# Optimization experiments

Measured on AMD Instinct MI355X. Metric: run time of the kernel, lower is better.

## Reference

```python
import jax, jax.numpy as jnp
import numpy as np

B, IDF, CDF, SIZE, H, L = 32, 64, 256, 32, 8, 256
SS = SIZE * SIZE  # size*size = 1024


def setup_inputs() -> dict:
    key = jax.random.key(0)
    k1, k2, k3 = jax.random.split(key, 3)
    return {
        "weightedContext": jax.random.normal(k1, (B, IDF, SS), dtype=jnp.float32),
        "context": jax.random.normal(k2, (B, CDF, L), dtype=jnp.float32),
        # per-head conv1x1 weights: [H, size*size, cdf]
        "W": jax.random.normal(k3, (H, SS, CDF), dtype=jnp.float32) * 0.02,
        "ih": SIZE,
        "iw": SIZE,
    }


def reference(weightedContext, context, W, ih, iw):
    batch, idf = weightedContext.shape[0], weightedContext.shape[1]
    # conv1x1 per head == per-head GEMM over channel dim: [B,H,SS,L]
    sourceC = jnp.einsum("hoc,bcl->bhol", W, context)
    # attention scores: [B,H,idf,L]
    attn = jnp.einsum("bio,bhol->bhil", weightedContext, sourceC)
    # softmax over sourceL (nn.Softmax() on 2D view -> dim=1 == L here)
    attn = jax.nn.softmax(attn, axis=-1)
    # weightedContext_T summed over heads: bmm(sourceC, attn^T) -> [B,idf,SS]
    ctx_out = jnp.einsum("bhol,bhil->bio", sourceC, attn)
    ctx_out = ctx_out.reshape(batch, idf, ih, iw)
    # attnOut: per-head attn transposed [B,L,idf], summed over heads
    attn_out = jnp.sum(attn, axis=1).transpose(0, 2, 1)
    return ctx_out, attn_out
```

## Files before the change

kernel.cpp:

```cpp
#include <hip/hip_runtime.h>
#include <hip/hip_bf16.h>

#define BB 32
#define IDF 64
#define CDF 256
#define SSZ 1024
#define NH 8
#define LL 256
#define KHC 2048

typedef __attribute__((ext_vector_type(8))) _Float16 half8v;
typedef __attribute__((ext_vector_type(4))) float f32x4;

#define GLDS16(g, l) __builtin_amdgcn_global_load_lds(                        \
    (const __attribute__((address_space(1))) void*)(g),                       \
    (__attribute__((address_space(3))) void*)(l), 16, 0, 0)

#define WAIT_ENTER3(NFULL, NHALF)                                             \
  { if (ks < NSTEP - 2)                                                       \
      asm volatile("s_waitcnt vmcnt(" #NFULL ")" ::: "memory");               \
    else if (ks == NSTEP - 2)                                                 \
      asm volatile("s_waitcnt vmcnt(" #NHALF ")" ::: "memory");               \
    else                                                                      \
      asm volatile("s_waitcnt vmcnt(0)" ::: "memory");                        \
    __builtin_amdgcn_s_barrier();                                             \
    __builtin_amdgcn_sched_barrier(0); }
#define BAR_EXIT()                                                            \
  { __builtin_amdgcn_sched_barrier(0);                                        \
    __builtin_amdgcn_s_barrier();                                             \
    __builtin_amdgcn_sched_barrier(0); }
#define LDS_BAR()                                                             \
  { asm volatile("s_waitcnt lgkmcnt(0)" ::: "memory");                        \
    __builtin_amdgcn_s_barrier();                                             \
    __builtin_amdgcn_sched_barrier(0); }

__device__ inline unsigned short f2h(float x) {
  _Float16 h = (_Float16)x;
  return *reinterpret_cast<unsigned short*>(&h);
}
__device__ inline float h2f(unsigned short u) {
  _Float16 h = *reinterpret_cast<_Float16*>(&u);
  return (float)h;
}

__global__ __launch_bounds__(256) void k_prep(const float* __restrict__ wc,
                                              const float* __restrict__ W,
                                              const float* __restrict__ ctx,
                                              unsigned short* __restrict__ wc16,
                                              unsigned short* __restrict__ W16,
                                              unsigned short* __restrict__ ctx16,
                                              unsigned short* __restrict__ Wt16,
                                              unsigned short* __restrict__ cT16) {
  __shared__ float Tt[64][65];
  int blk0 = blockIdx.x;
  int t = threadIdx.x;
  if (blk0 < 6144) {
    int sel = blk0 >> 11;
    int idx = ((blk0 & 2047) * 256 + t) * 4;
    const float* src = (sel == 0) ? wc : (sel == 1) ? W : ctx;
    unsigned short* d = (sel == 0) ? wc16 : (sel == 1) ? W16 : ctx16;
    float4 v = *reinterpret_cast<const float4*>(&src[idx]);
    __align__(8) unsigned short h[4] = {f2h(v.x), f2h(v.y), f2h(v.z), f2h(v.w)};
    *reinterpret_cast<int2*>(&d[idx]) = *reinterpret_cast<int2*>(h);
  } else if (blk0 < 6656) {
    int blk = blk0 - 6144;
    int h = blk >> 6, ot = (blk >> 2) & 15, cq = blk & 3;
    int og = ot * 64, cg = cq * 64;
    int o_l = t >> 4, c4 = (t & 15) * 4;
#pragma unroll
    for (int p = 0; p < 4; ++p) {
      int o = o_l + 16 * p;
      float4 v = *reinterpret_cast<const float4*>(
          &W[((size_t)h * SSZ + og + o) * CDF + cg + c4]);
      Tt[c4 + 0][o] = v.x; Tt[c4 + 1][o] = v.y;
      Tt[c4 + 2][o] = v.z; Tt[c4 + 3][o] = v.w;
    }
    __syncthreads();
    int c_l = t >> 2;
#pragma unroll
    for (int p = 0; p < 4; ++p) {
      int o0 = ((t & 3) + 4 * p) * 4;
      __align__(8) unsigned short hv[4];
#pragma unroll
      for (int j = 0; j < 4; ++j) hv[j] = f2h(Tt[c_l][o0 + j]);
      size_t base = ((size_t)h * CDF + cg + c_l) * SSZ + og + o0;
      *reinterpret_cast<int2*>(&Wt16[base]) = *reinterpret_cast<int2*>(hv);
    }
  } else {
    int blk = blk0 - 6656;
    int b = blk >> 4, cq = (blk >> 2) & 3, lt = blk & 3;
    int cg = cq * 64, lg = lt * 64;
    int c_l = t >> 4, l4 = (t & 15) * 4;
#pragma unroll
    for (int p = 0; p < 4; ++p) {
      int c = c_l + 16 * p;
      float4 v = *reinterpret_cast<const float4*>(
          &ctx[((size_t)b * CDF + cg + c) * LL + lg + l4]);
      Tt[l4 + 0][c] = v.x; Tt[l4 + 1][c] = v.y;
      Tt[l4 + 2][c] = v.z; Tt[l4 + 3][c] = v.w;
    }
    __syncthreads();
    int l_l = t >> 2;
#pragma unroll
    for (int p = 0; p < 4; ++p) {
      int c0 = ((t & 3) + 4 * p) * 4;
      __align__(8) unsigned short hv[4];
#pragma unroll
      for (int j = 0; j < 4; ++j) hv[j] = f2h(Tt[l_l][c0 + j]);
      size_t base = ((size_t)b * LL + lg + l_l) * CDF + cg + c0;
      *reinterpret_cast<int2*>(&cT16[base]) = *reinterpret_cast<int2*>(hv);
    }
  }
}

#define BUF_SH 10240

__device__ __forceinline__ void st_p1(short* dst, const short* gA, const short* gB,
                                      int wave, int lane, int k0) {
#pragma unroll
  for (int j = 0; j < 5; ++j) {
    int inst = wave * 5 + j;
    const short* src; int toff, rb;
    if (inst < 2)       { src = gA; toff = 0;    rb = inst * 16; }
    else if (inst < 18) { src = gB; toff = 1024; rb = (inst - 2) * 16; }
    else                { src = gA; toff = 9216; rb = (inst - 18) * 16; }
    int r  = rb + (lane >> 2);
    int gc = (lane & 3) ^ ((r >> 1) & 3);
    GLDS16(src + (size_t)r * SSZ + k0 + gc * 8, dst + toff + rb * 32);
  }
}
__device__ __forceinline__ void st_pB(short* dst, const short* gB, int ld,
                                      int wave, int lane, int k0) {
#pragma unroll
  for (int j = 0; j < 4; ++j) {
    int rb = (wave * 4 + j) * 16;
    int r  = rb + (lane >> 2);
    int gc = (lane & 3) ^ ((r >> 1) & 3);
    GLDS16(gB + (size_t)r * ld + k0 + gc * 8, dst + 1024 + rb * 32);
  }
}

__global__ __launch_bounds__(256) void k123(const unsigned short* __restrict__ wc16,
                                            const unsigned short* __restrict__ Wt16,
                                            const unsigned short* __restrict__ cT16,
                                            const unsigned short* __restrict__ ctx16,
                                            unsigned short* __restrict__ P16,
                                            unsigned short* __restrict__ N216) {
  __shared__ __align__(16) short S[3 * BUF_SH + 8192];
  short* P_lds = &S[3 * BUF_SH];

  int blk = blockIdx.x;
  int bh = blk >> 1, ih = blk & 1;
  int b = bh >> 3, h = bh & 7;
  int ibase = ih * 32;
  int t = threadIdx.x;
  int lane = t & 63, wave = t >> 6;
  int ln15 = lane & 15, kh = lane >> 4;
  int rowq = (lane >> 4) * 4;

  const short* gA = (const short*)wc16 + (size_t)(b * IDF + ibase) * SSZ;
  const short* gB = (const short*)Wt16 + (size_t)h * CDF * SSZ;
  const short* gT = (const short*)cT16 + (size_t)b * LL * CDF;
  const short* gC = (const short*)ctx16 + (size_t)b * CDF * LL;

  int offA[2], offB[4], rowM[2], rmask[2];
#pragma unroll
  for (int r = 0; r < 2; ++r) {
    int row = r * 16 + ln15;
    offA[r] = row * 32 + ((kh ^ ((row >> 1) & 3)) * 8);
    rowM[r] = row * 256;
    rmask[r] = row & 7;
  }
#pragma unroll
  for (int c = 0; c < 4; ++c) {
    int row = wave * 64 + c * 16 + ln15;
    offB[c] = 1024 + row * 32 + ((kh ^ ((row >> 1) & 3)) * 8);
  }

  f32x4 acc[2][4] = {};

  st_p1(&S[0],           gA, gB, wave, lane, 0);
  st_p1(&S[BUF_SH],      gA, gB, wave, lane, 32);
  st_p1(&S[2 * BUF_SH],  gA, gB, wave, lane, 64);
  int cur = 0;
  {
    const int NSTEP = 32;
#pragma unroll 1
    for (int ks = 0; ks < NSTEP; ++ks) {
      short* Sc = &S[cur * BUF_SH];
      WAIT_ENTER3(10, 5)
      half8v fa[2], fb[4];
#pragma unroll
      for (int r = 0; r < 2; ++r)
        fa[r] = *reinterpret_cast<const half8v*>(&Sc[offA[r]]);
#pragma unroll
      for (int c = 0; c < 4; ++c)
        fb[c] = *reinterpret_cast<const half8v*>(&Sc[offB[c]]);
      __builtin_amdgcn_s_setprio(1);
#pragma unroll
      for (int r = 0; r < 2; ++r)
#pragma unroll
        for (int c = 0; c < 4; ++c)
          acc[r][c] = __builtin_amdgcn_mfma_f32_16x16x32_f16(fa[r], fb[c], acc[r][c], 0, 0, 0);
      __builtin_amdgcn_s_setprio(0);
      BAR_EXIT()
      if (ks + 3 < NSTEP)
        st_p1(Sc, gA, gB, wave, lane, (ks + 3) * 32);
      cur = (cur == 2) ? 0 : cur + 1;
    }
  }
#pragma unroll
  for (int r = 0; r < 2; ++r)
#pragma unroll
    for (int c = 0; c < 4; ++c)
#pragma unroll
      for (int reg = 0; reg < 4; ++reg) {
        int row = r * 16 + rowq + reg;
        int col = wave * 64 + c * 16 + ln15;
        P_lds[row * 256 + ((((col >> 3) ^ (row & 7)) << 3) + (col & 7))] =
            (short)f2h(acc[r][c][reg]);
      }
  LDS_BAR()

#pragma unroll
  for (int r = 0; r < 2; ++r)
#pragma unroll
    for (int c = 0; c < 4; ++c) acc[r][c] = (f32x4){0.f, 0.f, 0.f, 0.f};
  st_pB(&S[0],          gT, CDF, wave, lane, 0);
  st_pB(&S[BUF_SH],     gT, CDF, wave, lane, 32);
  st_pB(&S[2 * BUF_SH], gT, CDF, wave, lane, 64);
  cur = 0;
  {
    const int NSTEP = 8;
#pragma unroll 1
    for (int ks = 0; ks < NSTEP; ++ks) {
      short* Sc = &S[cur * BUF_SH];
      WAIT_ENTER3(8, 4)
      half8v fa[2], fb[4];
#pragma unroll
      for (int r = 0; r < 2; ++r) {
        int ck = ((ks * 4 + kh) ^ rmask[r]) << 3;
        fa[r] = *reinterpret_cast<const half8v*>(&P_lds[rowM[r] + ck]);
      }
#pragma unroll
      for (int c = 0; c < 4; ++c)
        fb[c] = *reinterpret_cast<const half8v*>(&Sc[offB[c]]);
      __builtin_amdgcn_s_setprio(1);
#pragma unroll
      for (int r = 0; r < 2; ++r)
#pragma unroll
        for (int c = 0; c < 4; ++c)
          acc[r][c] = __builtin_amdgcn_mfma_f32_16x16x32_f16(fa[r], fb[c], acc[r][c], 0, 0, 0);
      __builtin_amdgcn_s_setprio(0);
      BAR_EXIT()
      if (ks + 3 < NSTEP)
        st_pB(Sc, gT, CDF, wave, lane, (ks + 3) * 32);
      cur = (cur == 2) ? 0 : cur + 1;
    }
  }

  st_pB(&S[0],          gC, LL, wave, lane, 0);
  st_pB(&S[BUF_SH],     gC, LL, wave, lane, 32);
  st_pB(&S[2 * BUF_SH], gC, LL, wave, lane, 64);

  float* pm = reinterpret_cast<float*>(P_lds);
  float gmax[2][4], ginv[2][4];
#pragma unroll
  for (int r = 0; r < 2; ++r)
#pragma unroll
    for (int reg = 0; reg < 4; ++reg) {
      float m = fmaxf(fmaxf(acc[r][0][reg], acc[r][1][reg]),
                      fmaxf(acc[r][2][reg], acc[r][3][reg]));
#pragma unroll
      for (int msk = 8; msk >= 1; msk >>= 1) m = fmaxf(m, __shfl_xor(m, msk, 64));
      if (ln15 == 0) pm[(r * 16 + rowq + reg) * 4 + wave] = m;
    }
  LDS_BAR()
#pragma unroll
  for (int r = 0; r < 2; ++r)
#pragma unroll
    for (int reg = 0; reg < 4; ++reg) {
      int row = r * 16 + rowq + reg;
      float4 p0 = *reinterpret_cast<const float4*>(&pm[row * 4]);
      gmax[r][reg] = fmaxf(fmaxf(p0.x, p0.y), fmaxf(p0.z, p0.w));
    }
  LDS_BAR()
#pragma unroll
  for (int r = 0; r < 2; ++r)
#pragma unroll
    for (int reg = 0; reg < 4; ++reg) {
      float s = 0.f;
#pragma unroll
      for (int c = 0; c < 4; ++c) {
        acc[r][c][reg] = __expf(acc[r][c][reg] - gmax[r][reg]);
        s += acc[r][c][reg];
      }
#pragma unroll
      for (int msk = 8; msk >= 1; msk >>= 1) s += __shfl_xor(s, msk, 64);
      if (ln15 == 0) pm[(r * 16 + rowq + reg) * 4 + wave] = s;
    }
  LDS_BAR()
#pragma unroll
  for (int r = 0; r < 2; ++r)
#pragma unroll
    for (int reg = 0; reg < 4; ++reg) {
      int row = r * 16 + rowq + reg;
      float4 p0 = *reinterpret_cast<const float4*>(&pm[row * 4]);
      ginv[r][reg] = 1.f / (p0.x + p0.y + p0.z + p0.w);
    }
  LDS_BAR()

  size_t pbase = (size_t)bh * IDF * LL + (size_t)ibase * LL;
#pragma unroll
  for (int r = 0; r < 2; ++r)
#pragma unroll
    for (int c = 0; c < 4; ++c)
#pragma unroll
      for (int reg = 0; reg < 4; ++reg) {
        float p = acc[r][c][reg] * ginv[r][reg];
        int row = r * 16 + rowq + reg;
        int col = wave * 64 + c * 16 + ln15;
        unsigned short ph = f2h(p);
        P16[pbase + (size_t)row * LL + col] = ph;
        P_lds[row * 256 + ((((col >> 3) ^ (row & 7)) << 3) + (col & 7))] = (short)ph;
      }
  LDS_BAR()

#pragma unroll
  for (int r = 0; r < 2; ++r)
#pragma unroll
    for (int c = 0; c < 4; ++c) acc[r][c] = (f32x4){0.f, 0.f, 0.f, 0.f};
  cur = 0;
  {
    const int NSTEP = 8;
#pragma unroll 1
    for (int ks = 0; ks < NSTEP; ++ks) {
      short* Sc = &S[cur * BUF_SH];
      WAIT_ENTER3(8, 4)
      half8v fa[2], fb[4];
#pragma unroll
      for (int r = 0; r < 2; ++r) {
        int ck = ((ks * 4 + kh) ^ rmask[r]) << 3;
        fa[r] = *reinterpret_cast<const half8v*>(&P_lds[rowM[r] + ck]);
      }
#pragma unroll
      for (int c = 0; c < 4; ++c)
        fb[c] = *reinterpret_cast<const half8v*>(&Sc[offB[c]]);
      __builtin_amdgcn_s_setprio(1);
#pragma unroll
      for (int r = 0; r < 2; ++r)
#pragma unroll
        for (int c = 0; c < 4; ++c)
          acc[r][c] = __builtin_amdgcn_mfma_f32_16x16x32_f16(fa[r], fb[c], acc[r][c], 0, 0, 0);
      __builtin_amdgcn_s_setprio(0);
      BAR_EXIT()
      if (ks + 3 < NSTEP)
        st_pB(Sc, gC, LL, wave, lane, (ks + 3) * 32);
      cur = (cur == 2) ? 0 : cur + 1;
    }
  }

  size_t nbase = (size_t)b * IDF * KHC + (size_t)ibase * KHC + h * CDF;
#pragma unroll
  for (int r = 0; r < 2; ++r)
#pragma unroll
    for (int c = 0; c < 4; ++c)
#pragma unroll
      for (int reg = 0; reg < 4; ++reg) {
        int row = r * 16 + rowq + reg;
        int col = wave * 64 + c * 16 + ln15;
        N216[nbase + (size_t)row * KHC + col] = f2h(acc[r][c][reg]);
      }
}

__device__ __forceinline__ void k4_stage(short* dst,
                                         const short* gA, const short* gB,
                                         int wave, int lane, int kk0, int obase) {
  int h4 = kk0 >> 8, cb = kk0 & 255;
#pragma unroll
  for (int j = 0; j < 3; ++j) {
    int inst = wave * 3 + j;
    if (inst < 4) {
      int rb = inst * 16;
      int r  = rb + (lane >> 2);
      int gc = (lane & 3) ^ ((r >> 1) & 3);
      GLDS16(gA + (size_t)r * KHC + kk0 + gc * 8, dst + rb * 32);
    } else {
      int rb = (inst - 4) * 16;
      int r  = rb + (lane >> 2);
      int gc = (lane & 3) ^ ((r >> 1) & 3);
      GLDS16(gB + (size_t)(h4 * SSZ + obase + r) * CDF + cb + gc * 8,
             dst + 2048 + rb * 32);
    }
  }
}

__global__ __launch_bounds__(256) void k4_mfma(const unsigned short* __restrict__ N216,
                                               const unsigned short* __restrict__ W16,
                                               float* __restrict__ out0,
                                               float* __restrict__ out1) {
  __shared__ __align__(16) short S[3 * 6144];

  int blk = blockIdx.x;
  int g = blk >> 8;
  int r8 = blk & 255;
  int b = r8 >> 3, ot = r8 & 7;
  int obase = ot * 128;
  int t = threadIdx.x;
  int lane = t & 63, wave = t >> 6;
  int ln15 = lane & 15, kh = lane >> 4;

  const short* gA = (const short*)N216 + (size_t)b * IDF * KHC;
  const short* gB = (const short*)W16;

  int offA[4], offB[2];
#pragma unroll
  for (int r = 0; r < 4; ++r) {
    int row = r * 16 + ln15;
    offA[r] = row * 32 + ((kh ^ ((row >> 1) & 3)) * 8);
  }
#pragma unroll
  for (int c = 0; c < 2; ++c) {
    int row = wave * 32 + c * 16 + ln15;
    offB[c] = 2048 + row * 32 + ((kh ^ ((row >> 1) & 3)) * 8);
  }

  int kbase = g * (KHC / 2);
  f32x4 acc[4][2] = {};

  k4_stage(&S[0],        gA, gB, wave, lane, kbase, obase);
  k4_stage(&S[6144],     gA, gB, wave, lane, kbase + 32, obase);
  k4_stage(&S[2 * 6144], gA, gB, wave, lane, kbase + 64, obase);
  int cur = 0;

  const int NSTEP = 32;
#pragma unroll 1
  for (int ks = 0; ks < NSTEP; ++ks) {
    short* Sc = &S[cur * 6144];
    WAIT_ENTER3(6, 3)
    half8v fa[4], fb[2];
#pragma unroll
    for (int r = 0; r < 4; ++r)
      fa[r] = *reinterpret_cast<const half8v*>(&Sc[offA[r]]);
#pragma unroll
    for (int c = 0; c < 2; ++c)
      fb[c] = *reinterpret_cast<const half8v*>(&Sc[offB[c]]);
    __builtin_amdgcn_s_setprio(1);
#pragma unroll
    for (int r = 0; r < 4; ++r)
#pragma unroll
      for (int c = 0; c < 2; ++c)
        acc[r][c] = __builtin_amdgcn_mfma_f32_16x16x32_f16(fa[r], fb[c], acc[r][c], 0, 0, 0);
    __builtin_amdgcn_s_setprio(0);
    BAR_EXIT()
    if (ks + 3 < NSTEP)
      k4_stage(Sc, gA, gB, wave, lane, kbase + (ks + 3) * 32, obase);
    cur = (cur == 2) ? 0 : cur + 1;
  }

  float* dst = (g == 0) ? out0 : out1;
  int rowq = (lane >> 4) * 4;
#pragma unroll
  for (int r = 0; r < 4; ++r)
#pragma unroll
    for (int c = 0; c < 2; ++c)
#pragma unroll
      for (int reg = 0; reg < 4; ++reg)
        dst[((size_t)b * IDF + r * 16 + rowq + reg) * SSZ +
            obase + wave * 32 + c * 16 + ln15] = acc[r][c][reg];
}

__global__ __launch_bounds__(256) void k_epi(const unsigned short* __restrict__ P16,
                                             float* __restrict__ outa,
                                             float* __restrict__ out,
                                             const float* __restrict__ Pbuf) {
  int blk0 = blockIdx.x;
  int tid = threadIdx.x;
  if (blk0 >= 128) {
    int idx = (blk0 - 128) * 256 + tid;
    float4 a = reinterpret_cast<float4*>(out)[idx];
    float4 p = reinterpret_cast<const float4*>(Pbuf)[idx];
    a.x += p.x; a.y += p.y; a.z += p.z; a.w += p.w;
    reinterpret_cast<float4*>(out)[idx] = a;
    return;
  }
  __shared__ float T[64][65];
  int b = blk0 >> 2, lt = blk0 & 3;
  int l0 = lt * 64;
  float4 acc[4];
#pragma unroll
  for (int p = 0; p < 4; ++p) acc[p] = make_float4(0.f, 0.f, 0.f, 0.f);
  for (int h = 0; h < NH; ++h) {
    size_t src = (size_t)(b * NH + h) * IDF * LL;
#pragma unroll
    for (int p = 0; p < 4; ++p) {
      int f = tid + p * 256;
      int i = f >> 4, lc = (f & 15) * 4;
      ushort4 u = *reinterpret_cast<const ushort4*>(&P16[src + i * LL + l0 + lc]);
      acc[p].x += h2f(u.x); acc[p].y += h2f(u.y);
      acc[p].z += h2f(u.z); acc[p].w += h2f(u.w);
    }
  }
#pragma unroll
  for (int p = 0; p < 4; ++p) {
    int f = tid + p * 256;
    int i = f >> 4, lc = (f & 15) * 4;
    T[i][lc + 0] = acc[p].x; T[i][lc + 1] = acc[p].y;
    T[i][lc + 2] = acc[p].z; T[i][lc + 3] = acc[p].w;
  }
  __syncthreads();
#pragma unroll
  for (int p = 0; p < 4; ++p) {
    int f = tid + p * 256;
    int lr = f >> 4, ic = (f & 15) * 4;
    float4 v = {T[ic + 0][lr], T[ic + 1][lr], T[ic + 2][lr], T[ic + 3][lr]};
    *reinterpret_cast<float4*>(&outa[((size_t)b * LL + l0 + lr) * IDF + ic]) = v;
  }
}

extern "C" void kernel_launch(void* const* d_in, const int* in_sizes, int n_in,
                              void* d_out, int out_size, void* d_ws, size_t ws_size,
                              hipStream_t stream) {
  const float* wc  = (const float*)d_in[0];
  const float* ctx = (const float*)d_in[1];
  const float* W   = (const float*)d_in[2];
  float* out = (float*)d_out;

  const size_t NE = 2097152;
  const size_t NM = 4194304;
  unsigned short* p = (unsigned short*)d_ws;
  unsigned short *wc16 = p;   p += NE;
  unsigned short *Wt16 = p;   p += NE;
  unsigned short *W16  = p;   p += NE;
  unsigned short *ctx16 = p;  p += NE;
  unsigned short *cT16 = p;   p += NE;
  unsigned short *P16  = p;   p += NM;
  unsigned short *N216 = p;   p += NM;
  float* Pbuf = (float*)p;

  k_prep  <<<7168, 256, 0, stream>>>(wc, W, ctx, wc16, W16, ctx16, Wt16, cT16);
  k123    <<<BB * NH * 2, 256, 0, stream>>>(wc16, Wt16, cT16, ctx16, P16, N216);
  k4_mfma <<<512, 256, 0, stream>>>(N216, W16, out, Pbuf);
  k_epi   <<<2176, 256, 0, stream>>>(P16, out + (size_t)BB * IDF * SSZ, out, Pbuf);
}
```

Before: 80.28 us.

## Share per-head W tile across two batches per 512-thread block in k123

k123 now processes two batch items for the same head and i-half in one 512-thread block. The two 4-wave groups share the LDS-staged W^T tile in phase 1, which halves W traffic per unit of work and halves the grid to 256 blocks. LDS use grows to roughly 128KB per block, which limits occupancy to one block per CU, and the larger barriers span 8 waves.

```diff
diff --git a/kernel.cpp b/kernel.cpp
--- a/kernel.cpp
+++ b/kernel.cpp
@@ -113,89 +113,109 @@
   }
 }
 
-#define BUF_SH 10240
-
-__device__ __forceinline__ void st_p1(short* dst, const short* gA, const short* gB,
-                                      int wave, int lane, int k0) {
-#pragma unroll
-  for (int j = 0; j < 5; ++j) {
-    int inst = wave * 5 + j;
-    const short* src; int toff, rb;
-    if (inst < 2)       { src = gA; toff = 0;    rb = inst * 16; }
-    else if (inst < 18) { src = gB; toff = 1024; rb = (inst - 2) * 16; }
-    else                { src = gA; toff = 9216; rb = (inst - 18) * 16; }
-    int r  = rb + (lane >> 2);
-    int gc = (lane & 3) ^ ((r >> 1) & 3);
-    GLDS16(src + (size_t)r * SSZ + k0 + gc * 8, dst + toff + rb * 32);
-  }
-}
-__device__ __forceinline__ void st_pB(short* dst, const short* gB, int ld,
-                                      int wave, int lane, int k0) {
+#define BUFS 16384
+
+__device__ __forceinline__ void st_p1(short* dst,
+                                      const short* gA0, const short* gA1,
+                                      const short* gB, int wave, int lane, int k0) {
+#pragma unroll
+  for (int j = 0; j < 3; ++j) {
+    int inst = wave * 3 + j;
+    if (inst < 4 || inst >= 20) {
+      int ai = (inst < 4) ? inst : (inst - 20);
+      const short* src = (ai < 2) ? gA0 : gA1;
+      int lr = (ai & 1) * 16 + (lane >> 2);
+      int gc = (lane & 3) ^ ((lr >> 1) & 3);
+      int toff = ((inst < 4) ? 0 : 10240) + ai * 512;
+      GLDS16(src + (size_t)lr * SSZ + k0 + gc * 8, dst + toff);
+    } else {
+      int bi = inst - 4;
+      int brow = bi * 16 + (lane >> 2);
+      int gc = (lane & 3) ^ ((brow >> 1) & 3);
+      GLDS16(gB + (size_t)brow * SSZ + k0 + gc * 8, dst + 2048 + bi * 512);
+    }
+  }
+}
+__device__ __forceinline__ void st_p23(short* dst,
+                                       const short* gB0, const short* gB1,
+                                       int ld, int wave, int lane, int k0) {
 #pragma unroll
   for (int j = 0; j < 4; ++j) {
-    int rb = (wave * 4 + j) * 16;
-    int r  = rb + (lane >> 2);
-    int gc = (lane & 3) ^ ((r >> 1) & 3);
-    GLDS16(gB + (size_t)r * ld + k0 + gc * 8, dst + 1024 + rb * 32);
-  }
-}
-
-__global__ __launch_bounds__(256) void k123(const unsigned short* __restrict__ wc16,
+    int inst = wave * 4 + j;
+    int g = inst >> 4;
+    int r16 = inst & 15;
+    int brow = r16 * 16 + (lane >> 2);
+    int gc = (lane & 3) ^ ((brow >> 1) & 3);
+    const short* src = g ? gB1 : gB0;
+    GLDS16(src + (size_t)brow * ld + k0 + gc * 8, dst + g * 8192 + r16 * 512);
+  }
+}
+
+__global__ __launch_bounds__(512) void k123(const unsigned short* __restrict__ wc16,
                                             const unsigned short* __restrict__ Wt16,
                                             const unsigned short* __restrict__ cT16,
                                             const unsigned short* __restrict__ ctx16,
                                             unsigned short* __restrict__ P16,
                                             unsigned short* __restrict__ N216) {
-  __shared__ __align__(16) short S[3 * BUF_SH + 8192];
-  short* P_lds = &S[3 * BUF_SH];
+  __shared__ __align__(16) short S[3 * BUFS + 16384];
+  short* P_lds = &S[3 * BUFS];
 
   int blk = blockIdx.x;
-  int bh = blk >> 1, ih = blk & 1;
-  int b = bh >> 3, h = bh & 7;
+  int h = blk & 7, ih = (blk >> 3) & 1, bp = blk >> 4;
   int ibase = ih * 32;
   int t = threadIdx.x;
   int lane = t & 63, wave = t >> 6;
+  int g = wave >> 2, w4 = wave & 3;
   int ln15 = lane & 15, kh = lane >> 4;
   int rowq = (lane >> 4) * 4;
 
-  const short* gA = (const short*)wc16 + (size_t)(b * IDF + ibase) * SSZ;
-  const short* gB = (const short*)Wt16 + (size_t)h * CDF * SSZ;
-  const short* gT = (const short*)cT16 + (size_t)b * LL * CDF;
-  const short* gC = (const short*)ctx16 + (size_t)b * CDF * LL;
-
-  int offA[2], offB[4], rowM[2], rmask[2];
+  int b_g = bp * 2 + g;
+  int bh_g = b_g * 8 + h;
+
+  const short* gA0 = (const short*)wc16 + (size_t)((bp * 2 + 0) * IDF + ibase) * SSZ;
+  const short* gA1 = (const short*)wc16 + (size_t)((bp * 2 + 1) * IDF + ibase) * SSZ;
+  const short* gB  = (const short*)Wt16 + (size_t)h * CDF * SSZ;
+  const short* gT0 = (const short*)cT16 + (size_t)(bp * 2 + 0) * LL * CDF;
+  const short* gT1 = (const short*)cT16 + (size_t)(bp * 2 + 1) * LL * CDF;
+  const short* gC0 = (const short*)ctx16 + (size_t)(bp * 2 + 0) * CDF * LL;
+  const short* gC1 = (const short*)ctx16 + (size_t)(bp * 2 + 1) * CDF * LL;
+
+  int offA[2], rowM[2], rmask[2];
 #pragma unroll
   for (int r = 0; r < 2; ++r) {
-    int row = r * 16 + ln15;
-    offA[r] = row * 32 + ((kh ^ ((row >> 1) & 3)) * 8);
-    rowM[r] = row * 256;
-    rmask[r] = row & 7;
-  }
+    int lr = r * 16 + ln15;
+    offA[r] = g * 1024 + lr * 32 + ((kh ^ ((lr >> 1) & 3)) * 8);
+    rowM[r] = g * 8192 + lr * 256;
+    rmask[r] = lr & 7;
+  }
+  int offB1[4], offB2[4];
 #pragma unroll
   for (int c = 0; c < 4; ++c) {
-    int row = wave * 64 + c * 16 + ln15;
-    offB[c] = 1024 + row * 32 + ((kh ^ ((row >> 1) & 3)) * 8);
+    int row = w4 * 64 + c * 16 + ln15;
+    int swz = ((kh ^ ((row >> 1) & 3)) * 8);
+    offB1[c] = 2048 + row * 32 + swz;
+    offB2[c] = g * 8192 + row * 32 + swz;
   }
 
   f32x4 acc[2][4] = {};
 
-  st_p1(&S[0],           gA, gB, wave, lane, 0);
-  st_p1(&S[BUF_SH],      gA, gB, wave, lane, 32);
-  st_p1(&S[2 * BUF_SH],  gA, gB, wave, lane, 64);
+  st_p1(&S[0],        gA0, gA1, gB, wave, lane, 0);
+  st_p1(&S[BUFS],     gA0, gA1, gB, wave, lane, 32);
+  st_p1(&S[2 * BUFS], gA0, gA1, gB, wave, lane, 64);
   int cur = 0;
   {
     const int NSTEP = 32;
 #pragma unroll 1
     for (int ks = 0; ks < NSTEP; ++ks) {
-      short* Sc = &S[cur * BUF_SH];
-      WAIT_ENTER3(10, 5)
+      short* Sc = &S[cur * BUFS];
+      WAIT_ENTER3(6, 3)
       half8v fa[2], fb[4];
 #pragma unroll
       for (int r = 0; r < 2; ++r)
         fa[r] = *reinterpret_cast<const half8v*>(&Sc[offA[r]]);
 #pragma unroll
       for (int c = 0; c < 4; ++c)
-        fb[c] = *reinterpret_cast<const half8v*>(&Sc[offB[c]]);
+        fb[c] = *reinterpret_cast<const half8v*>(&Sc[offB1[c]]);
       __builtin_amdgcn_s_setprio(1);
 #pragma unroll
       for (int r = 0; r < 2; ++r)
@@ -205,7 +225,7 @@
       __builtin_amdgcn_s_setprio(0);
       BAR_EXIT()
       if (ks + 3 < NSTEP)
-        st_p1(Sc, gA, gB, wave, lane, (ks + 3) * 32);
+        st_p1(Sc, gA0, gA1, gB, wave, lane, (ks + 3) * 32);
       cur = (cur == 2) ? 0 : cur + 1;
     }
   }
@@ -216,8 +236,9 @@
 #pragma unroll
       for (int reg = 0; reg < 4; ++reg) {
         int row = r * 16 + rowq + reg;
-        int col = wave * 64 + c * 16 + ln15;
-        P_lds[row * 256 + ((((col >> 3) ^ (row & 7)) << 3) + (col & 7))] =
+        int col = w4 * 64 + c * 16 + ln15;
+        P_lds[g * 8192 + row * 256 +
+              ((((col >> 3) ^ (row & 7)) << 3) + (col & 7))] =
             (short)f2h(acc[r][c][reg]);
       }
   LDS_BAR()
@@ -226,15 +247,15 @@
   for (int r = 0; r < 2; ++r)
 #pragma unroll
     for (int c = 0; c < 4; ++c) acc[r][c] = (f32x4){0.f, 0.f, 0.f, 0.f};
-  st_pB(&S[0],          gT, CDF, wave, lane, 0);
-  st_pB(&S[BUF_SH],     gT, CDF, wave, lane, 32);
-  st_pB(&S[2 * BUF_SH], gT, CDF, wave, lane, 64);
+  st_p23(&S[0],        gT0, gT1, CDF, wave, lane, 0);
+  st_p23(&S[BUFS],     gT0, gT1, CDF, wave, lane, 32);
+  st_p23(&S[2 * BUFS], gT0, gT1, CDF, wave, lane, 64);
   cur = 0;
   {
     const int NSTEP = 8;
 #pragma unroll 1
     for (int ks = 0; ks < NSTEP; ++ks) {
-      short* Sc = &S[cur * BUF_SH];
+      short* Sc = &S[cur * BUFS];
       WAIT_ENTER3(8, 4)
       half8v fa[2], fb[4];
 #pragma unroll
@@ -244,7 +265,7 @@
       }
 #pragma unroll
       for (int c = 0; c < 4; ++c)
-        fb[c] = *reinterpret_cast<const half8v*>(&Sc[offB[c]]);
+        fb[c] = *reinterpret_cast<const half8v*>(&Sc[offB2[c]]);
       __builtin_amdgcn_s_setprio(1);
 #pragma unroll
       for (int r = 0; r < 2; ++r)
@@ -254,16 +275,16 @@
       __builtin_amdgcn_s_setprio(0);
       BAR_EXIT()
       if (ks + 3 < NSTEP)
-        st_pB(Sc, gT, CDF, wave, lane, (ks + 3) * 32);
+        st_p23(Sc, gT0, gT1, CDF, wave, lane, (ks + 3) * 32);
       cur = (cur == 2) ? 0 : cur + 1;
     }
   }
 
-  st_pB(&S[0],          gC, LL, wave, lane, 0);
-  st_pB(&S[BUF_SH],     gC, LL, wave, lane, 32);
-  st_pB(&S[2 * BUF_SH], gC, LL, wave, lane, 64);
-
-  float* pm = reinterpret_cast<float*>(P_lds);
+  st_p23(&S[0],        gC0, gC1, LL, wave, lane, 0);
+  st_p23(&S[BUFS],     gC0, gC1, LL, wave, lane, 32);
+  st_p23(&S[2 * BUFS], gC0, gC1, LL, wave, lane, 64);
+
+  float* pm = reinterpret_cast<float*>(&P_lds[g * 8192]);
   float gmax[2][4], ginv[2][4];
 #pragma unroll
   for (int r = 0; r < 2; ++r)
@@ -273,7 +294,7 @@
                       fmaxf(acc[r][2][reg], acc[r][3][reg]));
 #pragma unroll
       for (int msk = 8; msk >= 1; msk >>= 1) m = fmaxf(m, __shfl_xor(m, msk, 64));
-      if (ln15 == 0) pm[(r * 16 + rowq + reg) * 4 + wave] = m;
+      if (ln15 == 0) pm[(r * 16 + rowq + reg) * 4 + w4] = m;
     }
   LDS_BAR()
 #pragma unroll
@@ -297,7 +318,7 @@
       }
 #pragma unroll
       for (int msk = 8; msk >= 1; msk >>= 1) s += __shfl_xor(s, msk, 64);
-      if (ln15 == 0) pm[(r * 16 + rowq + reg) * 4 + wave] = s;
+      if (ln15 == 0) pm[(r * 16 + rowq + reg) * 4 + w4] = s;
     }
   LDS_BAR()
 #pragma unroll
@@ -310,7 +331,7 @@
     }
   LDS_BAR()
 
-  size_t pbase = (size_t)bh * IDF * LL + (size_t)ibase * LL;
+  size_t pbase = (size_t)bh_g * IDF * LL + (size_t)ibase * LL;
 #pragma unroll
   for (int r = 0; r < 2; ++r)
 #pragma unroll
@@ -319,10 +340,11 @@
       for (int reg = 0; reg < 4; ++reg) {
         float p = acc[r][c][reg] * ginv[r][reg];
         int row = r * 16 + rowq + reg;
-        int col = wave * 64 + c * 16 + ln15;
+        int col = w4 * 64 + c * 16 + ln15;
         unsigned short ph = f2h(p);
         P16[pbase + (size_t)row * LL + col] = ph;
-        P_lds[row * 256 + ((((col >> 3) ^ (row & 7)) << 3) + (col & 7))] = (short)ph;
+        P_lds[g * 8192 + row * 256 +
+              ((((col >> 3) ^ (row & 7)) << 3) + (col & 7))] = (short)ph;
       }
   LDS_BAR()
 
@@ -335,7 +357,7 @@
     const int NSTEP = 8;
 #pragma unroll 1
     for (int ks = 0; ks < NSTEP; ++ks) {
-      short* Sc = &S[cur * BUF_SH];
+      short* Sc = &S[cur * BUFS];
       WAIT_ENTER3(8, 4)
       half8v fa[2], fb[4];
 #pragma unroll
@@ -345,7 +367,7 @@
       }
 #pragma unroll
       for (int c = 0; c < 4; ++c)
-        fb[c] = *reinterpret_cast<const half8v*>(&Sc[offB[c]]);
+        fb[c] = *reinterpret_cast<const half8v*>(&Sc[offB2[c]]);
       __builtin_amdgcn_s_setprio(1);
 #pragma unroll
       for (int r = 0; r < 2; ++r)
@@ -355,12 +377,12 @@
       __builtin_amdgcn_s_setprio(0);
       BAR_EXIT()
       if (ks + 3 < NSTEP)
-        st_pB(Sc, gC, LL, wave, lane, (ks + 3) * 32);
+        st_p23(Sc, gC0, gC1, LL, wave, lane, (ks + 3) * 32);
       cur = (cur == 2) ? 0 : cur + 1;
     }
   }
 
-  size_t nbase = (size_t)b * IDF * KHC + (size_t)ibase * KHC + h * CDF;
+  size_t nbase = (size_t)b_g * IDF * KHC + (size_t)ibase * KHC + h * CDF;
 #pragma unroll
   for (int r = 0; r < 2; ++r)
 #pragma unroll
@@ -368,7 +390,7 @@
 #pragma unroll
       for (int reg = 0; reg < 4; ++reg) {
         int row = r * 16 + rowq + reg;
-        int col = wave * 64 + c * 16 + ln15;
+        int col = w4 * 64 + c * 16 + ln15;
         N216[nbase + (size_t)row * KHC + col] = f2h(acc[r][c][reg]);
       }
 }
@@ -539,7 +561,7 @@
   float* Pbuf = (float*)p;
 
   k_prep  <<<7168, 256, 0, stream>>>(wc, W, ctx, wc16, W16, ctx16, Wt16, cT16);
-  k123    <<<BB * NH * 2, 256, 0, stream>>>(wc16, Wt16, cT16, ctx16, P16, N216);
+  k123    <<<256, 512, 0, stream>>>(wc16, Wt16, cT16, ctx16, P16, N216);
   k4_mfma <<<512, 256, 0, stream>>>(N216, W16, out, Pbuf);
   k_epi   <<<2176, 256, 0, stream>>>(P16, out + (size_t)BB * IDF * SSZ, out, Pbuf);
 }
```

Measured after the change: 78.21 us. 2.6% less time.
